# Kernel tuning notes

Hardware: AMD Instinct MI355X
Metric: run time of the kernel (lower is better)

The kernel has to match this reference:

```python
import jax, jax.numpy as jnp
import numpy as np

V = [642, 2562, 10242]
NGT = 8000
NSAMP = 4000
CHAM_W = [3000.0, 3000.0, 3000.0]
LAP_C = [0.2, 1.0, 1.0]
CHAM_OPP = 0.55
W_LAP, W_MOVE, W_EDGE, W_NORM = 1500.0, 50.0, 359.0, 0.5


def _normalize(x, axis=-1):
    n = jnp.linalg.norm(x, axis=axis, keepdims=True)
    return x / jnp.maximum(n, 1e-12)


def _mse(a, b):
    return jnp.mean((a - b) ** 2)


def _sample_points(verts, faces, n, key):
    # uniform face pick + uniform barycentric (sqrt trick), matches sample_point_cloud
    kf, kb = jax.random.split(key)
    fidx = jax.random.randint(kf, (n,), 0, faces.shape[0])
    tri = verts[faces[fidx]]  # [n,3,3]
    uv = jax.random.uniform(kb, (n, 2), dtype=verts.dtype)
    r1 = jnp.sqrt(uv[:, 0]); r2 = uv[:, 1]
    w = jnp.stack([1.0 - r1, r1 * (1.0 - r2), r1 * r2], axis=1)  # [n,3]
    return jnp.einsum('nk,nkd->nd', w, tri)


def _chamfer(gt, pred):
    # squared pairwise distances [B,Ng,Np]
    d = (jnp.sum(gt ** 2, -1)[:, :, None] + jnp.sum(pred ** 2, -1)[:, None, :]
         - 2.0 * jnp.einsum('bnd,bmd->bnm', gt, pred))
    dist1 = jnp.min(d, 2); idx1 = jnp.argmin(d, 2)  # gt -> nearest pred
    dist2 = jnp.min(d, 1); idx2 = jnp.argmin(d, 1)  # pred -> nearest gt
    return dist1, dist2, idx1, idx2


def _laplace_coord(x, lap):
    # x [B,n,3], lap [n,10]: 8 neighbor idx (-1 invalid), self idx, count
    idx = lap[:, :8]
    mask = idx < 0
    safe = jnp.where(mask, 0, idx)
    v = x[:, safe]  # [B,n,8,3]
    v = jnp.where(mask[None, :, :, None], 0.0, v)
    cnt = lap[:, -1].astype(x.dtype)
    return x - v.sum(2) / cnt[None, :, None]


def _block(gt, gtn, pred, pred_bef, lap, edges, faces, key, cham_w, lap_c, block_idx):
    samp = _sample_points(pred[0], faces, NSAMP, key)[None]
    sample_pred = jnp.concatenate([pred, samp], 1)
    d1, d2, _i1, i2 = _chamfer(gt, sample_pred)
    chamfer = cham_w * (jnp.mean(d1) + CHAM_OPP * jnp.mean(d2))
    e = _normalize(pred[:, edges[:, 0]] - pred[:, edges[:, 1]], 2)
    nn = jnp.take_along_axis(gtn, i2[..., None], axis=1)  # nearest gt normal per pred pt
    nrm = _normalize(nn[:, edges[:, 0]], 2)
    normal = jnp.mean(jnp.abs(jnp.sum(e * nrm, 2)))
    edge = _mse(pred[:, edges[:, 0]], pred[:, edges[:, 1]]) * 3.0
    lap_l = lap_c * _mse(_laplace_coord(pred_bef, lap), _laplace_coord(pred, lap)) * 3.0
    move = lap_c * _mse(pred_bef, pred) * 3.0 if block_idx > 0 else 0.0
    return chamfer, normal, edge, lap_l, move


def setup_inputs() -> dict:
    key = jax.random.key(0)
    ks = jax.random.split(key, 8)
    inp = {}
    inp['gt_points'] = jax.random.normal(ks[0], (1, NGT, 3), jnp.float32)
    inp['gt_normals'] = _normalize(jax.random.normal(ks[1], (1, NGT, 3), jnp.float32), 2)
    for i, v in enumerate(V):
        kp, kb, ke, kf, kl = jax.random.split(ks[2 + i], 5)
        pc = jax.random.normal(kp, (1, v, 3), jnp.float32)
        inp[f'pred_coord_{i}'] = pc
        inp[f'pred_before_{i}'] = pc + 0.1 * jax.random.normal(kb, (1, v, 3), jnp.float32)
        inp[f'edges_{i}'] = jax.random.randint(ke, (3 * v, 2), 0, v, dtype=jnp.int32)
        inp[f'faces_{i}'] = jax.random.randint(kf, (2 * v, 3), 0, v, dtype=jnp.int32)
        nbr = jax.random.randint(kl, (v, 8), 0, v, dtype=jnp.int32)
        valid = (nbr % 7) != 0
        valid = valid.at[:, 0].set(True)  # count >= 1
        cnt = valid.sum(1).astype(jnp.int32)
        nbr_m = jnp.where(valid, nbr, -1)
        self_idx = jnp.arange(v, dtype=jnp.int32)[:, None]
        inp[f'lap_idx_{i}'] = jnp.concatenate([nbr_m, self_idx, cnt[:, None]], 1)
    return inp


def reference(gt_points, gt_normals,
              pred_coord_0, pred_before_0, edges_0, faces_0, lap_idx_0,
              pred_coord_1, pred_before_1, edges_1, faces_1, lap_idx_1,
              pred_coord_2, pred_before_2, edges_2, faces_2, lap_idx_2):
    skey = jax.random.key(42)
    preds = [pred_coord_0, pred_coord_1, pred_coord_2]
    befs = [pred_before_0, pred_before_1, pred_before_2]
    edges = [edges_0, edges_1, edges_2]
    faces = [faces_0, faces_1, faces_2]
    laps = [lap_idx_0, lap_idx_1, lap_idx_2]
    ch = nl = el = ll = ml = 0.0
    for i in range(3):
        c, n, e, l, m = _block(gt_points, gt_normals, preds[i], befs[i], laps[i],
                               edges[i], faces[i], jax.random.fold_in(skey, i),
                               CHAM_W[i], LAP_C[i], i)
        ch += c; nl += n; el += e; ll += l; ml += m
    loss = ch + W_LAP * ll + W_MOVE * ml + W_EDGE * el + W_NORM * nl
    return loss
```

## Files before the change

kernel.cpp:

```cpp
#include <hip/hip_runtime.h>
#include <stdint.h>

#define NGT 8000
#define NSAMP 4000
#define QT 8
#define QB 2048
#define CH 128

struct Params {
  const float* gt;
  const float* gtn;
  const float* pred[3];
  const float* bef[3];
  const int*   edges[3];
  const int*   faces[3];
  const int*   lap[3];
  float* S[3];
  unsigned int* mb1[3];
  unsigned long long* mb2a[3];
  unsigned int* mb2b[3];
  float* acc;
  unsigned int* counter;
  unsigned int* init_base;
  int init_words;
  int prep_init_blocks;
  int v[3], M[3], E[3], F[3];
  int cseg[10];
  int cnc[9];
  int fseg[13];
};

__device__ __forceinline__ unsigned int ford(float f){
  unsigned int b = __float_as_uint(f);
  return b ^ ((b >> 31) ? 0xFFFFFFFFu : 0x80000000u);
}
__device__ __forceinline__ float funord(unsigned int u){
  unsigned int b = u ^ ((u >> 31) ? 0x80000000u : 0xFFFFFFFFu);
  return __uint_as_float(b);
}

__device__ __forceinline__ uint32_t rotl32(uint32_t x, int d){ return (x<<d)|(x>>(32-d)); }

__device__ __forceinline__ void tf2x32(uint32_t k0, uint32_t k1, uint32_t c0, uint32_t c1,
                                       uint32_t& o0, uint32_t& o1){
  uint32_t ks2 = k0 ^ k1 ^ 0x1BD11BDAu;
  uint32_t x0 = c0 + k0, x1 = c1 + k1;
  x0+=x1; x1=rotl32(x1,13); x1^=x0;
  x0+=x1; x1=rotl32(x1,15); x1^=x0;
  x0+=x1; x1=rotl32(x1,26); x1^=x0;
  x0+=x1; x1=rotl32(x1, 6); x1^=x0;
  x0+=k1; x1+=ks2+1u;
  x0+=x1; x1=rotl32(x1,17); x1^=x0;
  x0+=x1; x1=rotl32(x1,29); x1^=x0;
  x0+=x1; x1=rotl32(x1,16); x1^=x0;
  x0+=x1; x1=rotl32(x1,24); x1^=x0;
  x0+=ks2; x1+=k0+2u;
  x0+=x1; x1=rotl32(x1,13); x1^=x0;
  x0+=x1; x1=rotl32(x1,15); x1^=x0;
  x0+=x1; x1=rotl32(x1,26); x1^=x0;
  x0+=x1; x1=rotl32(x1, 6); x1^=x0;
  x0+=k0; x1+=k1+3u;
  x0+=x1; x1=rotl32(x1,17); x1^=x0;
  x0+=x1; x1=rotl32(x1,29); x1^=x0;
  x0+=x1; x1=rotl32(x1,16); x1^=x0;
  x0+=x1; x1=rotl32(x1,24); x1^=x0;
  x0+=k1; x1+=ks2+4u;
  x0+=x1; x1=rotl32(x1,13); x1^=x0;
  x0+=x1; x1=rotl32(x1,15); x1^=x0;
  x0+=x1; x1=rotl32(x1,26); x1^=x0;
  x0+=x1; x1=rotl32(x1, 6); x1^=x0;
  x0+=ks2; x1+=k0+5u;
  o0=x0; o1=x1;
}

__device__ __forceinline__ uint32_t rbits(uint32_t k0, uint32_t k1, uint32_t idx, uint32_t total){
  uint32_t half = total>>1, o0, o1;
  if (idx < half){ tf2x32(k0,k1, idx, idx+half, o0, o1); return o0; }
  tf2x32(k0,k1, idx-half, idx, o0, o1); return o1;
}

__global__ __launch_bounds__(256) void prep_kernel(Params p){
  int b = blockIdx.x;
  int t = threadIdx.x;
  if (b < p.prep_init_blocks){
    int wdi = b*256 + t;
    if (wdi < p.init_words)
      p.init_base[wdi] = (wdi < 64) ? 0u : 0xFFFFFFFFu;
    return;
  }
  int rem = b - p.prep_init_blocks;
  int i = rem >> 4;
  int s = ((rem & 15) << 8) + t;
  if (s >= NSAMP) return;
  uint32_t bk0, bk1; tf2x32(0u, 42u, 0u, (uint32_t)i, bk0, bk1);
  uint32_t ka0,kb0,ka1,kb1;
  tf2x32(bk0,bk1, 0u,2u, ka0,kb0);
  tf2x32(bk0,bk1, 1u,3u, ka1,kb1);
  uint32_t fb = rbits(ka0,ka1,(uint32_t)s, NSAMP);
  uint32_t fidx = fb % (uint32_t)p.F[i];
  uint32_t u0b = rbits(kb0,kb1, 2u*(uint32_t)s,    2u*NSAMP);
  uint32_t u1b = rbits(kb0,kb1, 2u*(uint32_t)s+1u, 2u*NSAMP);
  float u0 = __uint_as_float((u0b>>9)|0x3F800000u) - 1.0f;
  float u1 = __uint_as_float((u1b>>9)|0x3F800000u) - 1.0f;
  float r1 = sqrtf(u0);
  float w0 = 1.0f - r1, w1 = r1*(1.0f-u1), w2 = r1*u1;
  const int* f = p.faces[i] + 3*(int)fidx;
  const float* pr = p.pred[i];
  int va=f[0], vb=f[1], vc=f[2];
  float* dst = p.S[i] + 3*s;
  dst[0] = w0*pr[3*va+0] + w1*pr[3*vb+0] + w2*pr[3*vc+0];
  dst[1] = w0*pr[3*va+1] + w1*pr[3*vb+1] + w2*pr[3*vc+1];
  dst[2] = w0*pr[3*va+2] + w1*pr[3*vb+2] + w2*pr[3*vc+2];
}

__device__ __forceinline__ float dist_e(const float4 g, float qx, float qy, float qz){
  return fmaf(g.x,qx, fmaf(g.y,qy, fmaf(g.z,qz, g.w)));
}

__device__ __forceinline__ void scan_min(const float4* __restrict__ tile, int lim,
    const float* qx, const float* qy, const float* qz, float* best)
{
  int k = 0;
  int lim8 = lim & ~7;
  for (; k < lim8; k += 8){
    float4 g0=tile[k+0],g1=tile[k+1],g2=tile[k+2],g3=tile[k+3];
    float4 g4=tile[k+4],g5=tile[k+5],g6=tile[k+6],g7=tile[k+7];
    #pragma unroll
    for (int q=0;q<QT;q++){
      float d0=dist_e(g0,qx[q],qy[q],qz[q]);
      float d1=dist_e(g1,qx[q],qy[q],qz[q]);
      float d2=dist_e(g2,qx[q],qy[q],qz[q]);
      float d3=dist_e(g3,qx[q],qy[q],qz[q]);
      float d4=dist_e(g4,qx[q],qy[q],qz[q]);
      float d5=dist_e(g5,qx[q],qy[q],qz[q]);
      float d6=dist_e(g6,qx[q],qy[q],qz[q]);
      float d7=dist_e(g7,qx[q],qy[q],qz[q]);
      float m = fminf(fminf(best[q], d0), d1);
      m = fminf(fminf(m, d2), d3);
      m = fminf(fminf(m, d4), d5);
      m = fminf(fminf(m, d6), d7);
      best[q] = m;
    }
  }
  for (; k < lim; k++){
    float4 g = tile[k];
    #pragma unroll
    for (int q=0;q<QT;q++)
      best[q] = fminf(best[q], dist_e(g,qx[q],qy[q],qz[q]));
  }
}

__device__ __forceinline__ void scan_argmin(const float4* __restrict__ tile, int lim, int c0,
    const float* qx, const float* qy, const float* qz, float* best, int* bidx)
{
  int k = 0;
  int lim4 = lim & ~3;
  for (; k < lim4; k += 4){
    float4 g0=tile[k+0],g1=tile[k+1],g2=tile[k+2],g3=tile[k+3];
    #pragma unroll
    for (int q=0;q<QT;q++){
      float d0=dist_e(g0,qx[q],qy[q],qz[q]);
      float d1=dist_e(g1,qx[q],qy[q],qz[q]);
      float d2=dist_e(g2,qx[q],qy[q],qz[q]);
      float d3=dist_e(g3,qx[q],qy[q],qz[q]);
      if (d0 < best[q]){ best[q]=d0; bidx[q]=c0+k+0; }
      if (d1 < best[q]){ best[q]=d1; bidx[q]=c0+k+1; }
      if (d2 < best[q]){ best[q]=d2; bidx[q]=c0+k+2; }
      if (d3 < best[q]){ best[q]=d3; bidx[q]=c0+k+3; }
    }
  }
  for (; k < lim; k++){
    float4 g = tile[k];
    #pragma unroll
    for (int q=0;q<QT;q++){
      float d = dist_e(g,qx[q],qy[q],qz[q]);
      if (d < best[q]){ best[q]=d; bidx[q]=c0+k; }
    }
  }
}

__global__ __launch_bounds__(256) void chamfer_kernel(Params p){
  __shared__ float4 tile[CH];
  int b = blockIdx.x;
  int seg = 0;
  #pragma unroll
  for (int s=1;s<9;s++) seg += (b >= p.cseg[s]) ? 1 : 0;
  int rem  = b - p.cseg[seg];
  int nc   = p.cnc[seg];
  int cq   = rem / nc;
  int cc   = rem - cq*nc;
  int role = seg / 3;
  int i    = seg - role*3;
  int t = threadIdx.x;
  int qbase = cq*QB;
  int c0 = cc*CH;
  int v = p.v[i];

  if (role == 0){
    int M = p.M[i];
    int lim = min(M - c0, CH);
    if (t < lim){
      int j = c0 + t;
      const float* src = (j < v) ? (p.pred[i] + 3*j) : (p.S[i] + 3*(j-v));
      float x=src[0], y=src[1], z=src[2];
      tile[t] = make_float4(x,y,z, x*x+y*y+z*z);
    }
    float qx[QT],qy[QT],qz[QT],qs[QT],best[QT];
    #pragma unroll
    for (int k=0;k<QT;k++){
      int q = qbase + t + k*256;
      float x=0.f,y=0.f,z=0.f;
      if (q < NGT){ x=p.gt[3*q]; y=p.gt[3*q+1]; z=p.gt[3*q+2]; }
      qs[k]=x*x+y*y+z*z; qx[k]=-2.f*x; qy[k]=-2.f*y; qz[k]=-2.f*z;
      best[k]=3.4e38f;
    }
    __syncthreads();
    scan_min(tile, lim, qx,qy,qz,best);
    #pragma unroll
    for (int k=0;k<QT;k++){
      int q = qbase + t + k*256;
      if (q < NGT) atomicMin(&p.mb1[i][q], ford(best[k]+qs[k]));
    }
  } else if (role == 1){
    int lim = min(NGT - c0, CH);
    if (t < lim){
      int j = c0 + t;
      float x=p.gt[3*j], y=p.gt[3*j+1], z=p.gt[3*j+2];
      tile[t] = make_float4(x,y,z, x*x+y*y+z*z);
    }
    float qx[QT],qy[QT],qz[QT],qs[QT],best[QT];
    int bidx[QT];
    #pragma unroll
    for (int k=0;k<QT;k++){
      int q = qbase + t + k*256;
      float x=0.f,y=0.f,z=0.f;
      if (q < v){
        const float* src = p.pred[i] + 3*q;
        x=src[0]; y=src[1]; z=src[2];
      }
      qs[k]=x*x+y*y+z*z; qx[k]=-2.f*x; qy[k]=-2.f*y; qz[k]=-2.f*z;
      best[k]=3.4e38f; bidx[k]=0;
    }
    __syncthreads();
    scan_argmin(tile, lim, c0, qx,qy,qz,best,bidx);
    #pragma unroll
    for (int k=0;k<QT;k++){
      int q = qbase + t + k*256;
      if (q < v){
        unsigned long long pk = ((unsigned long long)ford(best[k]+qs[k])<<32) | (unsigned int)bidx[k];
        atomicMin(&p.mb2a[i][q], pk);
      }
    }
  } else {
    int lim = min(NGT - c0, CH);
    if (t < lim){
      int j = c0 + t;
      float x=p.gt[3*j], y=p.gt[3*j+1], z=p.gt[3*j+2];
      tile[t] = make_float4(x,y,z, x*x+y*y+z*z);
    }
    float qx[QT],qy[QT],qz[QT],qs[QT],best[QT];
    #pragma unroll
    for (int k=0;k<QT;k++){
      int q = qbase + t + k*256;
      float x=0.f,y=0.f,z=0.f;
      if (q < NSAMP){
        const float* src = p.S[i] + 3*q;
        x=src[0]; y=src[1]; z=src[2];
      }
      qs[k]=x*x+y*y+z*z; qx[k]=-2.f*x; qy[k]=-2.f*y; qz[k]=-2.f*z;
      best[k]=3.4e38f;
    }
    __syncthreads();
    scan_min(tile, lim, qx,qy,qz,best);
    #pragma unroll
    for (int k=0;k<QT;k++){
      int q = qbase + t + k*256;
      if (q < NSAMP) atomicMin(&p.mb2b[i][q], ford(best[k]+qs[k]));
    }
  }
}

__global__ __launch_bounds__(256) void finish_kernel(Params p, float* out){
  __shared__ float red[256];
  int b = blockIdx.x;
  int seg = 0;
  #pragma unroll
  for (int s=1;s<12;s++) seg += (b >= p.fseg[s]) ? 1 : 0;
  int rem = b - p.fseg[seg];
  int z = seg / 3;
  int i = seg - 3*z;
  int tid = threadIdx.x;
  int gidx = rem*256 + tid;

  if (z == 0){
    int M = p.M[i], v = p.v[i];
    float val = 0.f;
    if (gidx < M){
      if (gidx < v) val = funord((unsigned int)(p.mb2a[i][gidx]>>32));
      else          val = funord(p.mb2b[i][gidx-v]);
    }
    red[tid] = val; __syncthreads();
    for (int s=128;s>0;s>>=1){ if (tid<s) red[tid]+=red[tid+s]; __syncthreads(); }
    if (tid==0 && red[0]!=0.f) atomicAdd(&p.acc[8*i+1], red[0]);
  } else if (z == 1){
    float val = 0.f;
    if (gidx < NGT) val = funord(p.mb1[i][gidx]);
    red[tid] = val; __syncthreads();
    for (int s=128;s>0;s>>=1){ if (tid<s) red[tid]+=red[tid+s]; __syncthreads(); }
    if (tid==0 && red[0]!=0.f) atomicAdd(&p.acc[8*i+0], red[0]);
  } else if (z == 2){
    int E = p.E[i];
    float sq = 0.f, ad = 0.f;
    if (gidx < E){
      int e0 = p.edges[i][2*gidx], e1 = p.edges[i][2*gidx+1];
      const float* pr = p.pred[i];
      float dx = pr[3*e0+0]-pr[3*e1+0];
      float dy = pr[3*e0+1]-pr[3*e1+1];
      float dz = pr[3*e0+2]-pr[3*e1+2];
      sq = dx*dx+dy*dy+dz*dz;
      float inv = 1.0f / fmaxf(sqrtf(sq), 1e-12f);
      int g = (int)(unsigned int)p.mb2a[i][e0];
      float nx = p.gtn[3*g+0], ny = p.gtn[3*g+1], nz = p.gtn[3*g+2];
      float invg = 1.0f / fmaxf(sqrtf(nx*nx+ny*ny+nz*nz), 1e-12f);
      ad = fabsf((dx*nx+dy*ny+dz*nz)*inv*invg);
    }
    red[tid] = ad; __syncthreads();
    for (int s=128;s>0;s>>=1){ if (tid<s) red[tid]+=red[tid+s]; __syncthreads(); }
    if (tid==0 && red[0]!=0.f) atomicAdd(&p.acc[8*i+2], red[0]);
    __syncthreads();
    red[tid] = sq; __syncthreads();
    for (int s=128;s>0;s>>=1){ if (tid<s) red[tid]+=red[tid+s]; __syncthreads(); }
    if (tid==0 && red[0]!=0.f) atomicAdd(&p.acc[8*i+3], red[0]);
  } else {
    int v = p.v[i];
    float lsq = 0.f, msq = 0.f;
    if (gidx < v){
      const int* L = p.lap[i] + 10*gidx;
      const float* B = p.bef[i];
      const float* R = p.pred[i];
      float cnt = (float)L[9];
      float sb0=0,sb1=0,sb2=0, sp0=0,sp1=0,sp2=0;
      #pragma unroll
      for (int k=0;k<8;k++){
        int id = L[k];
        if (id >= 0){
          sb0 += B[3*id+0]; sb1 += B[3*id+1]; sb2 += B[3*id+2];
          sp0 += R[3*id+0]; sp1 += R[3*id+1]; sp2 += R[3*id+2];
        }
      }
      float lb0 = B[3*gidx+0] - sb0/cnt, lb1 = B[3*gidx+1] - sb1/cnt, lb2 = B[3*gidx+2] - sb2/cnt;
      float lp0 = R[3*gidx+0] - sp0/cnt, lp1 = R[3*gidx+1] - sp1/cnt, lp2 = R[3*gidx+2] - sp2/cnt;
      float d0=lb0-lp0, d1=lb1-lp1, d2=lb2-lp2;
      lsq = d0*d0+d1*d1+d2*d2;
      float m0=B[3*gidx+0]-R[3*gidx+0], m1=B[3*gidx+1]-R[3*gidx+1], m2=B[3*gidx+2]-R[3*gidx+2];
      msq = m0*m0+m1*m1+m2*m2;
    }
    red[tid] = lsq; __syncthreads();
    for (int s=128;s>0;s>>=1){ if (tid<s) red[tid]+=red[tid+s]; __syncthreads(); }
    if (tid==0 && red[0]!=0.f) atomicAdd(&p.acc[8*i+4], red[0]);
    __syncthreads();
    red[tid] = msq; __syncthreads();
    for (int s=128;s>0;s>>=1){ if (tid<s) red[tid]+=red[tid+s]; __syncthreads(); }
    if (tid==0 && red[0]!=0.f) atomicAdd(&p.acc[8*i+5], red[0]);
  }

  __syncthreads();
  if (tid == 0){
    __threadfence();
    unsigned int total = gridDim.x;
    unsigned int old = atomicAdd(p.counter, 1u);
    if (old == total-1){
      __threadfence();
      const float CHAMW[3] = {3000.0f, 3000.0f, 3000.0f};
      const float LAPC[3]  = {0.2f, 1.0f, 1.0f};
      float loss = 0.0f;
      for (int m=0;m<3;m++){
        float a0 = __hip_atomic_load(&p.acc[8*m+0], __ATOMIC_RELAXED, __HIP_MEMORY_SCOPE_AGENT);
        float a1 = __hip_atomic_load(&p.acc[8*m+1], __ATOMIC_RELAXED, __HIP_MEMORY_SCOPE_AGENT);
        float a2 = __hip_atomic_load(&p.acc[8*m+2], __ATOMIC_RELAXED, __HIP_MEMORY_SCOPE_AGENT);
        float a3 = __hip_atomic_load(&p.acc[8*m+3], __ATOMIC_RELAXED, __HIP_MEMORY_SCOPE_AGENT);
        float a4 = __hip_atomic_load(&p.acc[8*m+4], __ATOMIC_RELAXED, __HIP_MEMORY_SCOPE_AGENT);
        float a5 = __hip_atomic_load(&p.acc[8*m+5], __ATOMIC_RELAXED, __HIP_MEMORY_SCOPE_AGENT);
        float ch = CHAMW[m]*(a0/(float)NGT + 0.55f*a1/(float)p.M[m]);
        float nl = a2/(float)p.E[m];
        float el = a3/(float)p.E[m];
        float ll = LAPC[m]*a4/(float)p.v[m];
        float ml = (m>0) ? LAPC[m]*a5/(float)p.v[m] : 0.0f;
        loss += ch + 1500.0f*ll + 50.0f*ml + 359.0f*el + 0.5f*nl;
      }
      out[0] = loss;
    }
  }
}

extern "C" void kernel_launch(void* const* d_in, const int* in_sizes, int n_in,
                              void* d_out, int out_size, void* d_ws, size_t ws_size,
                              hipStream_t stream) {
  Params p;
  p.gt  = (const float*)d_in[0];
  p.gtn = (const float*)d_in[1];
  for (int i=0;i<3;i++){
    p.pred[i]  = (const float*)d_in[2+5*i];
    p.bef[i]   = (const float*)d_in[3+5*i];
    p.edges[i] = (const int*)  d_in[4+5*i];
    p.faces[i] = (const int*)  d_in[5+5*i];
    p.lap[i]   = (const int*)  d_in[6+5*i];
    p.v[i] = in_sizes[2+5*i]/3;
    p.E[i] = in_sizes[4+5*i]/2;
    p.F[i] = in_sizes[5+5*i]/3;
    p.M[i] = p.v[i] + NSAMP;
  }
  unsigned int* base = (unsigned int*)d_ws;
  p.acc = (float*)base;
  p.counter = base + 32;
  p.init_base = base;
  unsigned int* w = base + 64;
  for (int i=0;i<3;i++){ p.mb1[i]  = w; w += NGT; }
  for (int i=0;i<3;i++){ p.mb2a[i] = (unsigned long long*)w; w += 2*p.v[i]; }
  for (int i=0;i<3;i++){ p.mb2b[i] = w; w += NSAMP; }
  p.init_words = (int)(w - base);
  for (int i=0;i<3;i++){ p.S[i] = (float*)w; w += NSAMP*3; }

  int cnq[9];
  for (int i=0;i<3;i++){
    cnq[0+i] = (NGT + QB-1)/QB;           p.cnc[0+i] = (p.M[i] + CH-1)/CH;
    cnq[3+i] = (p.v[i] + QB-1)/QB;        p.cnc[3+i] = (NGT + CH-1)/CH;
    cnq[6+i] = (NSAMP + QB-1)/QB;         p.cnc[6+i] = (NGT + CH-1)/CH;
  }
  p.cseg[0] = 0;
  for (int s=0;s<9;s++) p.cseg[s+1] = p.cseg[s] + cnq[s]*p.cnc[s];

  int fn[12];
  for (int i=0;i<3;i++){
    fn[0+i] = (p.M[i] + 255)/256;
    fn[3+i] = (NGT + 255)/256;
    fn[6+i] = (p.E[i] + 255)/256;
    fn[9+i] = (p.v[i] + 255)/256;
  }
  p.fseg[0] = 0;
  for (int s=0;s<12;s++) p.fseg[s+1] = p.fseg[s] + fn[s];

  int initB = (p.init_words + 255)/256;
  p.prep_init_blocks = initB;

  prep_kernel   <<<dim3(initB + 3*16), 256, 0, stream>>>(p);
  chamfer_kernel<<<dim3(p.cseg[9]),    256, 0, stream>>>(p);
  finish_kernel <<<dim3(p.fseg[12]),   256, 0, stream>>>(p, (float*)d_out);
}
```

Baseline: 152.1 us.

## Replace chamfer atomicMin reductions with per-block partial buffers and a reduce kernel

Each chamfer block now writes its partial minima (or packed distance/index) to a dedicated slot in workspace instead of issuing global atomicMin. A new reduce kernel takes the min across chunks per query and folds the sum into the accumulators, which also removes the min-buffer init and two finish-kernel segments. The chunk size rises from 128 to 160, giving fewer partials per query. This trades atomic contention and init work for an extra kernel launch and more global-memory traffic, and it falls back to the old path when the workspace is too small.

```diff
diff --git a/kernel.cpp b/kernel.cpp
--- a/kernel.cpp
+++ b/kernel.cpp
@@ -5,7 +5,7 @@
 #define NSAMP 4000
 #define QT 8
 #define QB 2048
-#define CH 128
+#define CH 160
 
 struct Params {
   const float* gt;
@@ -16,6 +16,9 @@
   const int*   faces[3];
   const int*   lap[3];
   float* S[3];
+  float* pf;
+  unsigned long long* pu;
+  unsigned int* gidx[3];
   unsigned int* mb1[3];
   unsigned long long* mb2a[3];
   unsigned int* mb2b[3];
@@ -24,9 +27,11 @@
   unsigned int* init_base;
   int init_words;
   int prep_init_blocks;
+  int part;
   int v[3], M[3], E[3], F[3];
   int cseg[10];
   int cnc[9];
+  int rseg[10];
   int fseg[13];
 };
 
@@ -179,6 +184,7 @@
   }
 }
 
+template<int PART>
 __global__ __launch_bounds__(256) void chamfer_kernel(Params p){
   __shared__ float4 tile[CH];
   int b = blockIdx.x;
@@ -216,10 +222,19 @@
     }
     __syncthreads();
     scan_min(tile, lim, qx,qy,qz,best);
-    #pragma unroll
-    for (int k=0;k<QT;k++){
-      int q = qbase + t + k*256;
-      if (q < NGT) atomicMin(&p.mb1[i][q], ford(best[k]+qs[k]));
+    if (PART){
+      float* dst = p.pf + (size_t)b*2048;
+      #pragma unroll
+      for (int k=0;k<QT;k++){
+        int q = qbase + t + k*256;
+        if (q < NGT) dst[t + k*256] = best[k]+qs[k];
+      }
+    } else {
+      #pragma unroll
+      for (int k=0;k<QT;k++){
+        int q = qbase + t + k*256;
+        if (q < NGT) atomicMin(&p.mb1[i][q], ford(best[k]+qs[k]));
+      }
     }
   } else if (role == 1){
     int lim = min(NGT - c0, CH);
@@ -243,12 +258,24 @@
     }
     __syncthreads();
     scan_argmin(tile, lim, c0, qx,qy,qz,best,bidx);
-    #pragma unroll
-    for (int k=0;k<QT;k++){
-      int q = qbase + t + k*256;
-      if (q < v){
-        unsigned long long pk = ((unsigned long long)ford(best[k]+qs[k])<<32) | (unsigned int)bidx[k];
-        atomicMin(&p.mb2a[i][q], pk);
+    if (PART){
+      unsigned long long* dst = p.pu + (size_t)(b - p.cseg[3])*2048;
+      #pragma unroll
+      for (int k=0;k<QT;k++){
+        int q = qbase + t + k*256;
+        if (q < v){
+          unsigned long long pk = ((unsigned long long)ford(best[k]+qs[k])<<32) | (unsigned int)bidx[k];
+          dst[t + k*256] = pk;
+        }
+      }
+    } else {
+      #pragma unroll
+      for (int k=0;k<QT;k++){
+        int q = qbase + t + k*256;
+        if (q < v){
+          unsigned long long pk = ((unsigned long long)ford(best[k]+qs[k])<<32) | (unsigned int)bidx[k];
+          atomicMin(&p.mb2a[i][q], pk);
+        }
       }
     }
   } else {
@@ -272,12 +299,69 @@
     }
     __syncthreads();
     scan_min(tile, lim, qx,qy,qz,best);
-    #pragma unroll
-    for (int k=0;k<QT;k++){
-      int q = qbase + t + k*256;
-      if (q < NSAMP) atomicMin(&p.mb2b[i][q], ford(best[k]+qs[k]));
-    }
-  }
+    if (PART){
+      int nu = p.cseg[6] - p.cseg[3];
+      float* dst = p.pf + (size_t)(b - nu)*2048;
+      #pragma unroll
+      for (int k=0;k<QT;k++){
+        int q = qbase + t + k*256;
+        if (q < NSAMP) dst[t + k*256] = best[k]+qs[k];
+      }
+    } else {
+      #pragma unroll
+      for (int k=0;k<QT;k++){
+        int q = qbase + t + k*256;
+        if (q < NSAMP) atomicMin(&p.mb2b[i][q], ford(best[k]+qs[k]));
+      }
+    }
+  }
+}
+
+__global__ __launch_bounds__(256) void reduce_kernel(Params p){
+  __shared__ float red[256];
+  int b = blockIdx.x;
+  int seg = 0;
+  #pragma unroll
+  for (int s=1;s<9;s++) seg += (b >= p.rseg[s]) ? 1 : 0;
+  int rem = b - p.rseg[seg];
+  int role = seg / 3;
+  int i = seg - 3*role;
+  int t = threadIdx.x;
+  int q = rem*256 + t;
+  int cq = q >> 11, slot = q & 2047;
+  float val = 0.f;
+
+  if (role == 0){
+    int nc = p.cnc[i];
+    const float* src = p.pf + (size_t)(p.cseg[i] + cq*nc)*2048 + slot;
+    float m = 3.4e38f;
+    for (int cc=0; cc<nc; cc++) m = fminf(m, src[(size_t)cc*2048]);
+    if (q < NGT) val = m;
+  } else if (role == 1){
+    int nc = p.cnc[3+i];
+    const unsigned long long* src = p.pu + (size_t)(p.cseg[3+i] - p.cseg[3] + cq*nc)*2048 + slot;
+    unsigned long long m = ~0ull;
+    for (int cc=0; cc<nc; cc++){
+      unsigned long long x = src[(size_t)cc*2048];
+      if (x < m) m = x;
+    }
+    if (q < p.v[i]){
+      p.gidx[i][q] = (unsigned int)m;
+      val = funord((unsigned int)(m >> 32));
+    }
+  } else {
+    int nc = p.cnc[6+i];
+    int nu = p.cseg[6] - p.cseg[3];
+    const float* src = p.pf + (size_t)(p.cseg[6+i] + cq*nc - nu)*2048 + slot;
+    float m = 3.4e38f;
+    for (int cc=0; cc<nc; cc++) m = fminf(m, src[(size_t)cc*2048]);
+    if (q < NSAMP) val = m;
+  }
+
+  red[t] = val; __syncthreads();
+  for (int s=128;s>0;s>>=1){ if (t<s) red[t]+=red[t+s]; __syncthreads(); }
+  if (t==0 && red[0]!=0.f)
+    atomicAdd(&p.acc[8*i + ((role==0)?0:1)], red[0]);
 }
 
 __global__ __launch_bounds__(256) void finish_kernel(Params p, float* out){
@@ -319,7 +403,7 @@
       float dz = pr[3*e0+2]-pr[3*e1+2];
       sq = dx*dx+dy*dy+dz*dz;
       float inv = 1.0f / fmaxf(sqrtf(sq), 1e-12f);
-      int g = (int)(unsigned int)p.mb2a[i][e0];
+      int g = p.part ? (int)p.gidx[i][e0] : (int)(unsigned int)p.mb2a[i][e0];
       float nx = p.gtn[3*g+0], ny = p.gtn[3*g+1], nz = p.gtn[3*g+2];
       float invg = 1.0f / fmaxf(sqrtf(nx*nx+ny*ny+nz*nz), 1e-12f);
       ad = fabsf((dx*nx+dy*ny+dz*nz)*inv*invg);
@@ -410,30 +494,63 @@
     p.F[i] = in_sizes[5+5*i]/3;
     p.M[i] = p.v[i] + NSAMP;
   }
+
+  int cnq[9];
+  for (int i=0;i<3;i++){
+    cnq[0+i] = (NGT + QB-1)/QB;           p.cnc[0+i] = (p.M[i] + CH-1)/CH;
+    cnq[3+i] = (p.v[i] + QB-1)/QB;        p.cnc[3+i] = (NGT + CH-1)/CH;
+    cnq[6+i] = (NSAMP + QB-1)/QB;         p.cnc[6+i] = (NGT + CH-1)/CH;
+  }
+  p.cseg[0] = 0;
+  for (int s=0;s<9;s++) p.cseg[s+1] = p.cseg[s] + cnq[s]*p.cnc[s];
+  int nu = p.cseg[6] - p.cseg[3];
+  int nf = p.cseg[3] + (p.cseg[9] - p.cseg[6]);
+
+  size_t part_words = 64
+      + (size_t)(p.v[0]+p.v[1]+p.v[2])
+      + (size_t)3*NSAMP*3
+      + 2
+      + (size_t)nu*2048*2
+      + (size_t)nf*2048;
+  int part = (ws_size >= (part_words + 64)*sizeof(unsigned int)) ? 1 : 0;
+  p.part = part;
+
   unsigned int* base = (unsigned int*)d_ws;
   p.acc = (float*)base;
   p.counter = base + 32;
   p.init_base = base;
   unsigned int* w = base + 64;
-  for (int i=0;i<3;i++){ p.mb1[i]  = w; w += NGT; }
-  for (int i=0;i<3;i++){ p.mb2a[i] = (unsigned long long*)w; w += 2*p.v[i]; }
-  for (int i=0;i<3;i++){ p.mb2b[i] = w; w += NSAMP; }
-  p.init_words = (int)(w - base);
-  for (int i=0;i<3;i++){ p.S[i] = (float*)w; w += NSAMP*3; }
-
-  int cnq[9];
+  p.pf = nullptr; p.pu = nullptr;
+  for (int i=0;i<3;i++){ p.gidx[i]=nullptr; p.mb1[i]=nullptr; p.mb2a[i]=nullptr; p.mb2b[i]=nullptr; }
+
+  if (part){
+    for (int i=0;i<3;i++){ p.gidx[i] = w; w += p.v[i]; }
+    for (int i=0;i<3;i++){ p.S[i] = (float*)w; w += NSAMP*3; }
+    if ((w - base) & 1) w++;
+    p.pu = (unsigned long long*)w; w += (size_t)nu*2048*2;
+    p.pf = (float*)w;              w += (size_t)nf*2048;
+    p.init_words = 64;
+  } else {
+    for (int i=0;i<3;i++){ p.mb1[i]  = w; w += NGT; }
+    for (int i=0;i<3;i++){ p.mb2a[i] = (unsigned long long*)w; w += 2*p.v[i]; }
+    for (int i=0;i<3;i++){ p.mb2b[i] = w; w += NSAMP; }
+    p.init_words = (int)(w - base);
+    for (int i=0;i<3;i++){ p.S[i] = (float*)w; w += NSAMP*3; }
+  }
+
+  int rn[9];
   for (int i=0;i<3;i++){
-    cnq[0+i] = (NGT + QB-1)/QB;           p.cnc[0+i] = (p.M[i] + CH-1)/CH;
-    cnq[3+i] = (p.v[i] + QB-1)/QB;        p.cnc[3+i] = (NGT + CH-1)/CH;
-    cnq[6+i] = (NSAMP + QB-1)/QB;         p.cnc[6+i] = (NGT + CH-1)/CH;
-  }
-  p.cseg[0] = 0;
-  for (int s=0;s<9;s++) p.cseg[s+1] = p.cseg[s] + cnq[s]*p.cnc[s];
+    rn[0+i] = (NGT + 255)/256;
+    rn[3+i] = (p.v[i] + 255)/256;
+    rn[6+i] = (NSAMP + 255)/256;
+  }
+  p.rseg[0] = 0;
+  for (int s=0;s<9;s++) p.rseg[s+1] = p.rseg[s] + rn[s];
 
   int fn[12];
   for (int i=0;i<3;i++){
-    fn[0+i] = (p.M[i] + 255)/256;
-    fn[3+i] = (NGT + 255)/256;
+    fn[0+i] = part ? 0 : (p.M[i] + 255)/256;
+    fn[3+i] = part ? 0 : (NGT + 255)/256;
     fn[6+i] = (p.E[i] + 255)/256;
     fn[9+i] = (p.v[i] + 255)/256;
   }
@@ -443,7 +560,12 @@
   int initB = (p.init_words + 255)/256;
   p.prep_init_blocks = initB;
 
-  prep_kernel   <<<dim3(initB + 3*16), 256, 0, stream>>>(p);
-  chamfer_kernel<<<dim3(p.cseg[9]),    256, 0, stream>>>(p);
-  finish_kernel <<<dim3(p.fseg[12]),   256, 0, stream>>>(p, (float*)d_out);
-}
+  prep_kernel<<<dim3(initB + 3*16), 256, 0, stream>>>(p);
+  if (part){
+    chamfer_kernel<1><<<dim3(p.cseg[9]), 256, 0, stream>>>(p);
+    reduce_kernel  <<<dim3(p.rseg[9]),   256, 0, stream>>>(p);
+  } else {
+    chamfer_kernel<0><<<dim3(p.cseg[9]), 256, 0, stream>>>(p);
+  }
+  finish_kernel<<<dim3(p.fseg[12]), 256, 0, stream>>>(p, (float*)d_out);
+}
```

New measurement: 171.1 us. +12.5%, slower.

## Use packed FP32 FMA and min3 in chamfer scans with SoA tiles

Applied to the files above, without the earlier changes.

Switches the shared-memory candidate tile from an array of float4 to four separate x/y/z/norm arrays, so pairs of candidates can be loaded as float2. Distances are then computed two at a time with v_pk_fma_f32, and min reduction uses v_min3_f32, roughly halving the VALU instruction count in the inner loop. The tile size grows from 128 to 160 and launch bounds now request 4 blocks per CU. The changes add register pressure from the duplicated query vectors, and CH depends on host-side segment counts (cnc/cseg), which must match the new value.

```diff
diff --git a/kernel.cpp b/kernel.cpp
--- a/kernel.cpp
+++ b/kernel.cpp
@@ -5,7 +5,9 @@
 #define NSAMP 4000
 #define QT 8
 #define QB 2048
-#define CH 128
+#define CH 160
+
+typedef float f32x2 __attribute__((ext_vector_type(2)));
 
 struct Params {
   const float* gt;
@@ -37,6 +39,17 @@
 __device__ __forceinline__ float funord(unsigned int u){
   unsigned int b = u ^ ((u >> 31) ? 0x80000000u : 0xFFFFFFFFu);
   return __uint_as_float(b);
+}
+
+__device__ __forceinline__ f32x2 pk_fma(f32x2 a, f32x2 b, f32x2 c){
+  f32x2 d;
+  asm("v_pk_fma_f32 %0, %1, %2, %3" : "=v"(d) : "v"(a), "v"(b), "v"(c));
+  return d;
+}
+__device__ __forceinline__ float min3f(float a, float b, float c){
+  float d;
+  asm("v_min3_f32 %0, %1, %2, %3" : "=v"(d) : "v"(a), "v"(b), "v"(c));
+  return d;
 }
 
 __device__ __forceinline__ uint32_t rotl32(uint32_t x, int d){ return (x<<d)|(x>>(32-d)); }
@@ -113,74 +126,100 @@
   dst[2] = w0*pr[3*va+2] + w1*pr[3*vb+2] + w2*pr[3*vc+2];
 }
 
-__device__ __forceinline__ float dist_e(const float4 g, float qx, float qy, float qz){
-  return fmaf(g.x,qx, fmaf(g.y,qy, fmaf(g.z,qz, g.w)));
-}
-
-__device__ __forceinline__ void scan_min(const float4* __restrict__ tile, int lim,
-    const float* qx, const float* qy, const float* qz, float* best)
+
+__device__ __forceinline__ void scan_min_pk(
+    const float* sx, const float* sy, const float* sz, const float* ss, int lim,
+    const f32x2* qx2, const f32x2* qy2, const f32x2* qz2, float* best)
 {
-  int k = 0;
-  int lim8 = lim & ~7;
-  for (; k < lim8; k += 8){
-    float4 g0=tile[k+0],g1=tile[k+1],g2=tile[k+2],g3=tile[k+3];
-    float4 g4=tile[k+4],g5=tile[k+5],g6=tile[k+6],g7=tile[k+7];
-    #pragma unroll
-    for (int q=0;q<QT;q++){
-      float d0=dist_e(g0,qx[q],qy[q],qz[q]);
-      float d1=dist_e(g1,qx[q],qy[q],qz[q]);
-      float d2=dist_e(g2,qx[q],qy[q],qz[q]);
-      float d3=dist_e(g3,qx[q],qy[q],qz[q]);
-      float d4=dist_e(g4,qx[q],qy[q],qz[q]);
-      float d5=dist_e(g5,qx[q],qy[q],qz[q]);
-      float d6=dist_e(g6,qx[q],qy[q],qz[q]);
-      float d7=dist_e(g7,qx[q],qy[q],qz[q]);
-      float m = fminf(fminf(best[q], d0), d1);
-      m = fminf(fminf(m, d2), d3);
-      m = fminf(fminf(m, d4), d5);
-      m = fminf(fminf(m, d6), d7);
-      best[q] = m;
-    }
-  }
-  for (; k < lim; k++){
-    float4 g = tile[k];
-    #pragma unroll
-    for (int q=0;q<QT;q++)
-      best[q] = fminf(best[q], dist_e(g,qx[q],qy[q],qz[q]));
-  }
-}
-
-__device__ __forceinline__ void scan_argmin(const float4* __restrict__ tile, int lim, int c0,
-    const float* qx, const float* qy, const float* qz, float* best, int* bidx)
+  int np = lim >> 1;
+  int m = 0;
+  int np4 = np & ~3;
+  for (; m < np4; m += 4){
+    f32x2 gx0=*(const f32x2*)(sx+2*m),   gx1=*(const f32x2*)(sx+2*m+2),
+          gx2=*(const f32x2*)(sx+2*m+4), gx3=*(const f32x2*)(sx+2*m+6);
+    f32x2 gy0=*(const f32x2*)(sy+2*m),   gy1=*(const f32x2*)(sy+2*m+2),
+          gy2=*(const f32x2*)(sy+2*m+4), gy3=*(const f32x2*)(sy+2*m+6);
+    f32x2 gz0=*(const f32x2*)(sz+2*m),   gz1=*(const f32x2*)(sz+2*m+2),
+          gz2=*(const f32x2*)(sz+2*m+4), gz3=*(const f32x2*)(sz+2*m+6);
+    f32x2 gs0=*(const f32x2*)(ss+2*m),   gs1=*(const f32x2*)(ss+2*m+2),
+          gs2=*(const f32x2*)(ss+2*m+4), gs3=*(const f32x2*)(ss+2*m+6);
+    #pragma unroll
+    for (int q=0;q<QT;q++){
+      f32x2 a0 = pk_fma(gx0, qx2[q], pk_fma(gy0, qy2[q], pk_fma(gz0, qz2[q], gs0)));
+      f32x2 a1 = pk_fma(gx1, qx2[q], pk_fma(gy1, qy2[q], pk_fma(gz1, qz2[q], gs1)));
+      f32x2 a2 = pk_fma(gx2, qx2[q], pk_fma(gy2, qy2[q], pk_fma(gz2, qz2[q], gs2)));
+      f32x2 a3 = pk_fma(gx3, qx2[q], pk_fma(gy3, qy2[q], pk_fma(gz3, qz2[q], gs3)));
+      float b0 = min3f(best[q], a0.x, a0.y);
+      float b1 = min3f(b0,      a1.x, a1.y);
+      float b2 = min3f(b1,      a2.x, a2.y);
+      best[q]  = min3f(b2,      a3.x, a3.y);
+    }
+  }
+  for (; m < np; m++){
+    f32x2 gx=*(const f32x2*)(sx+2*m), gy=*(const f32x2*)(sy+2*m),
+          gz=*(const f32x2*)(sz+2*m), gs=*(const f32x2*)(ss+2*m);
+    #pragma unroll
+    for (int q=0;q<QT;q++){
+      f32x2 a = pk_fma(gx, qx2[q], pk_fma(gy, qy2[q], pk_fma(gz, qz2[q], gs)));
+      best[q] = min3f(best[q], a.x, a.y);
+    }
+  }
+  if (lim & 1){
+    int j = lim - 1;
+    float gx=sx[j], gy=sy[j], gz=sz[j], gs=ss[j];
+    #pragma unroll
+    for (int q=0;q<QT;q++){
+      float d = fmaf(gx,qx2[q].x, fmaf(gy,qy2[q].x, fmaf(gz,qz2[q].x, gs)));
+      best[q] = fminf(best[q], d);
+    }
+  }
+}
+
+__device__ __forceinline__ void scan_argmin_pk(
+    const float* sx, const float* sy, const float* sz, const float* ss, int lim, int c0,
+    const f32x2* qx2, const f32x2* qy2, const f32x2* qz2, float* best, int* bidx)
 {
-  int k = 0;
-  int lim4 = lim & ~3;
-  for (; k < lim4; k += 4){
-    float4 g0=tile[k+0],g1=tile[k+1],g2=tile[k+2],g3=tile[k+3];
-    #pragma unroll
-    for (int q=0;q<QT;q++){
-      float d0=dist_e(g0,qx[q],qy[q],qz[q]);
-      float d1=dist_e(g1,qx[q],qy[q],qz[q]);
-      float d2=dist_e(g2,qx[q],qy[q],qz[q]);
-      float d3=dist_e(g3,qx[q],qy[q],qz[q]);
-      if (d0 < best[q]){ best[q]=d0; bidx[q]=c0+k+0; }
-      if (d1 < best[q]){ best[q]=d1; bidx[q]=c0+k+1; }
-      if (d2 < best[q]){ best[q]=d2; bidx[q]=c0+k+2; }
-      if (d3 < best[q]){ best[q]=d3; bidx[q]=c0+k+3; }
-    }
-  }
-  for (; k < lim; k++){
-    float4 g = tile[k];
-    #pragma unroll
-    for (int q=0;q<QT;q++){
-      float d = dist_e(g,qx[q],qy[q],qz[q]);
-      if (d < best[q]){ best[q]=d; bidx[q]=c0+k; }
-    }
-  }
-}
-
-__global__ __launch_bounds__(256) void chamfer_kernel(Params p){
-  __shared__ float4 tile[CH];
+  int np = lim >> 1;
+  int m = 0;
+  int np2 = np & ~1;
+  for (; m < np2; m += 2){
+    f32x2 gx0=*(const f32x2*)(sx+2*m), gx1=*(const f32x2*)(sx+2*m+2);
+    f32x2 gy0=*(const f32x2*)(sy+2*m), gy1=*(const f32x2*)(sy+2*m+2);
+    f32x2 gz0=*(const f32x2*)(sz+2*m), gz1=*(const f32x2*)(sz+2*m+2);
+    f32x2 gs0=*(const f32x2*)(ss+2*m), gs1=*(const f32x2*)(ss+2*m+2);
+    #pragma unroll
+    for (int q=0;q<QT;q++){
+      f32x2 a0 = pk_fma(gx0, qx2[q], pk_fma(gy0, qy2[q], pk_fma(gz0, qz2[q], gs0)));
+      f32x2 a1 = pk_fma(gx1, qx2[q], pk_fma(gy1, qy2[q], pk_fma(gz1, qz2[q], gs1)));
+      if (a0.x < best[q]){ best[q]=a0.x; bidx[q]=c0+2*m+0; }
+      if (a0.y < best[q]){ best[q]=a0.y; bidx[q]=c0+2*m+1; }
+      if (a1.x < best[q]){ best[q]=a1.x; bidx[q]=c0+2*m+2; }
+      if (a1.y < best[q]){ best[q]=a1.y; bidx[q]=c0+2*m+3; }
+    }
+  }
+  for (; m < np; m++){
+    f32x2 gx=*(const f32x2*)(sx+2*m), gy=*(const f32x2*)(sy+2*m),
+          gz=*(const f32x2*)(sz+2*m), gs=*(const f32x2*)(ss+2*m);
+    #pragma unroll
+    for (int q=0;q<QT;q++){
+      f32x2 a = pk_fma(gx, qx2[q], pk_fma(gy, qy2[q], pk_fma(gz, qz2[q], gs)));
+      if (a.x < best[q]){ best[q]=a.x; bidx[q]=c0+2*m+0; }
+      if (a.y < best[q]){ best[q]=a.y; bidx[q]=c0+2*m+1; }
+    }
+  }
+  if (lim & 1){
+    int j = lim - 1;
+    float gx=sx[j], gy=sy[j], gz=sz[j], gs=ss[j];
+    #pragma unroll
+    for (int q=0;q<QT;q++){
+      float d = fmaf(gx,qx2[q].x, fmaf(gy,qy2[q].x, fmaf(gz,qz2[q].x, gs)));
+      if (d < best[q]){ best[q]=d; bidx[q]=c0+j; }
+    }
+  }
+}
+
+__global__ __launch_bounds__(256, 4) void chamfer_kernel(Params p){
+  __shared__ __align__(16) float sx[CH], sy[CH], sz[CH], ss[CH];
   int b = blockIdx.x;
   int seg = 0;
   #pragma unroll
@@ -203,19 +242,22 @@
       int j = c0 + t;
       const float* src = (j < v) ? (p.pred[i] + 3*j) : (p.S[i] + 3*(j-v));
       float x=src[0], y=src[1], z=src[2];
-      tile[t] = make_float4(x,y,z, x*x+y*y+z*z);
-    }
-    float qx[QT],qy[QT],qz[QT],qs[QT],best[QT];
+      sx[t]=x; sy[t]=y; sz[t]=z; ss[t]=x*x+y*y+z*z;
+    }
+    f32x2 qx2[QT],qy2[QT],qz2[QT];
+    float qs[QT],best[QT];
     #pragma unroll
     for (int k=0;k<QT;k++){
       int q = qbase + t + k*256;
       float x=0.f,y=0.f,z=0.f;
       if (q < NGT){ x=p.gt[3*q]; y=p.gt[3*q+1]; z=p.gt[3*q+2]; }
-      qs[k]=x*x+y*y+z*z; qx[k]=-2.f*x; qy[k]=-2.f*y; qz[k]=-2.f*z;
+      qs[k]=x*x+y*y+z*z;
+      float ax=-2.f*x, ay=-2.f*y, az=-2.f*z;
+      qx2[k]=f32x2{ax,ax}; qy2[k]=f32x2{ay,ay}; qz2[k]=f32x2{az,az};
       best[k]=3.4e38f;
     }
     __syncthreads();
-    scan_min(tile, lim, qx,qy,qz,best);
+    scan_min_pk(sx,sy,sz,ss, lim, qx2,qy2,qz2, best);
     #pragma unroll
     for (int k=0;k<QT;k++){
       int q = qbase + t + k*256;
@@ -226,9 +268,10 @@
     if (t < lim){
       int j = c0 + t;
       float x=p.gt[3*j], y=p.gt[3*j+1], z=p.gt[3*j+2];
-      tile[t] = make_float4(x,y,z, x*x+y*y+z*z);
-    }
-    float qx[QT],qy[QT],qz[QT],qs[QT],best[QT];
+      sx[t]=x; sy[t]=y; sz[t]=z; ss[t]=x*x+y*y+z*z;
+    }
+    f32x2 qx2[QT],qy2[QT],qz2[QT];
+    float qs[QT],best[QT];
     int bidx[QT];
     #pragma unroll
     for (int k=0;k<QT;k++){
@@ -238,11 +281,13 @@
         const float* src = p.pred[i] + 3*q;
         x=src[0]; y=src[1]; z=src[2];
       }
-      qs[k]=x*x+y*y+z*z; qx[k]=-2.f*x; qy[k]=-2.f*y; qz[k]=-2.f*z;
+      qs[k]=x*x+y*y+z*z;
+      float ax=-2.f*x, ay=-2.f*y, az=-2.f*z;
+      qx2[k]=f32x2{ax,ax}; qy2[k]=f32x2{ay,ay}; qz2[k]=f32x2{az,az};
       best[k]=3.4e38f; bidx[k]=0;
     }
     __syncthreads();
-    scan_argmin(tile, lim, c0, qx,qy,qz,best,bidx);
+    scan_argmin_pk(sx,sy,sz,ss, lim, c0, qx2,qy2,qz2, best, bidx);
     #pragma unroll
     for (int k=0;k<QT;k++){
       int q = qbase + t + k*256;
@@ -256,9 +301,10 @@
     if (t < lim){
       int j = c0 + t;
       float x=p.gt[3*j], y=p.gt[3*j+1], z=p.gt[3*j+2];
-      tile[t] = make_float4(x,y,z, x*x+y*y+z*z);
-    }
-    float qx[QT],qy[QT],qz[QT],qs[QT],best[QT];
+      sx[t]=x; sy[t]=y; sz[t]=z; ss[t]=x*x+y*y+z*z;
+    }
+    f32x2 qx2[QT],qy2[QT],qz2[QT];
+    float qs[QT],best[QT];
     #pragma unroll
     for (int k=0;k<QT;k++){
       int q = qbase + t + k*256;
@@ -267,11 +313,13 @@
         const float* src = p.S[i] + 3*q;
         x=src[0]; y=src[1]; z=src[2];
       }
-      qs[k]=x*x+y*y+z*z; qx[k]=-2.f*x; qy[k]=-2.f*y; qz[k]=-2.f*z;
+      qs[k]=x*x+y*y+z*z;
+      float ax=-2.f*x, ay=-2.f*y, az=-2.f*z;
+      qx2[k]=f32x2{ax,ax}; qy2[k]=f32x2{ay,ay}; qz2[k]=f32x2{az,az};
       best[k]=3.4e38f;
     }
     __syncthreads();
-    scan_min(tile, lim, qx,qy,qz,best);
+    scan_min_pk(sx,sy,sz,ss, lim, qx2,qy2,qz2, best);
     #pragma unroll
     for (int k=0;k<QT;k++){
       int q = qbase + t + k*256;
```

Measured after the change: 160.6 us. 5.6% more time.

## Prepack points as padded float4 with norms and scan from global memory

Applied to the files above, without the earlier changes.

The prep kernel now writes padded float4 arrays (xyz plus squared norm) for ground-truth and predicted-plus-sampled points. Padding entries carry a huge norm so they never win the minimum. The chamfer kernel drops its shared-memory tile and __syncthreads and reads these packed arrays straight from global memory, where every thread loads the same addresses. The chunk size grows from 128 to 192 and the scan loop runs a fixed length with no tail loop. In exchange it adds workspace, extra prep work and more redundant global/L1 loads per thread.

```diff
diff --git a/kernel.cpp b/kernel.cpp
--- a/kernel.cpp
+++ b/kernel.cpp
@@ -2,10 +2,12 @@
 #include <stdint.h>
 
 #define NGT 8000
+#define NGTPAD 8064
+#define NCGT 42
 #define NSAMP 4000
 #define QT 8
 #define QB 2048
-#define CH 128
+#define CH 192
 
 struct Params {
   const float* gt;
@@ -16,6 +18,8 @@
   const int*   faces[3];
   const int*   lap[3];
   float* S[3];
+  float* gtpk;
+  float* Ppk[3];
   unsigned int* mb1[3];
   unsigned long long* mb2a[3];
   unsigned int* mb2b[3];
@@ -25,6 +29,8 @@
   int init_words;
   int prep_init_blocks;
   int v[3], M[3], E[3], F[3];
+  int padM[3];
+  int ppB[3];
   int cseg[10];
   int cnc[9];
   int fseg[13];
@@ -88,9 +94,41 @@
       p.init_base[wdi] = (wdi < 64) ? 0u : 0xFFFFFFFFu;
     return;
   }
-  int rem = b - p.prep_init_blocks;
-  int i = rem >> 4;
-  int s = ((rem & 15) << 8) + t;
+  b -= p.prep_init_blocks;
+  if (b < 32){
+    int idx = b*256 + t;
+    if (idx < NGTPAD){
+      float4 o;
+      if (idx < NGT){
+        float x=p.gt[3*idx], y=p.gt[3*idx+1], z=p.gt[3*idx+2];
+        o = make_float4(x,y,z, x*x+y*y+z*z);
+      } else {
+        o = make_float4(0.f,0.f,0.f,3.4e38f);
+      }
+      ((float4*)p.gtpk)[idx] = o;
+    }
+    return;
+  }
+  b -= 32;
+  #pragma unroll
+  for (int i=0;i<3;i++){
+    if (b < p.ppB[i]){
+      int idx = b*256 + t;
+      if (idx < p.padM[i]){
+        int v = p.v[i];
+        if (idx < v){
+          float x=p.pred[i][3*idx], y=p.pred[i][3*idx+1], z=p.pred[i][3*idx+2];
+          ((float4*)p.Ppk[i])[idx] = make_float4(x,y,z, x*x+y*y+z*z);
+        } else if (idx >= v + NSAMP){
+          ((float4*)p.Ppk[i])[idx] = make_float4(0.f,0.f,0.f,3.4e38f);
+        }
+      }
+      return;
+    }
+    b -= p.ppB[i];
+  }
+  int i = b >> 4;
+  int s = ((b & 15) << 8) + t;
   if (s >= NSAMP) return;
   uint32_t bk0, bk1; tf2x32(0u, 42u, 0u, (uint32_t)i, bk0, bk1);
   uint32_t ka0,kb0,ka1,kb1;
@@ -107,80 +145,16 @@
   const int* f = p.faces[i] + 3*(int)fidx;
   const float* pr = p.pred[i];
   int va=f[0], vb=f[1], vc=f[2];
+  float d0 = w0*pr[3*va+0] + w1*pr[3*vb+0] + w2*pr[3*vc+0];
+  float d1 = w0*pr[3*va+1] + w1*pr[3*vb+1] + w2*pr[3*vc+1];
+  float d2 = w0*pr[3*va+2] + w1*pr[3*vb+2] + w2*pr[3*vc+2];
   float* dst = p.S[i] + 3*s;
-  dst[0] = w0*pr[3*va+0] + w1*pr[3*vb+0] + w2*pr[3*vc+0];
-  dst[1] = w0*pr[3*va+1] + w1*pr[3*vb+1] + w2*pr[3*vc+1];
-  dst[2] = w0*pr[3*va+2] + w1*pr[3*vb+2] + w2*pr[3*vc+2];
-}
-
-__device__ __forceinline__ float dist_e(const float4 g, float qx, float qy, float qz){
-  return fmaf(g.x,qx, fmaf(g.y,qy, fmaf(g.z,qz, g.w)));
-}
-
-__device__ __forceinline__ void scan_min(const float4* __restrict__ tile, int lim,
-    const float* qx, const float* qy, const float* qz, float* best)
-{
-  int k = 0;
-  int lim8 = lim & ~7;
-  for (; k < lim8; k += 8){
-    float4 g0=tile[k+0],g1=tile[k+1],g2=tile[k+2],g3=tile[k+3];
-    float4 g4=tile[k+4],g5=tile[k+5],g6=tile[k+6],g7=tile[k+7];
-    #pragma unroll
-    for (int q=0;q<QT;q++){
-      float d0=dist_e(g0,qx[q],qy[q],qz[q]);
-      float d1=dist_e(g1,qx[q],qy[q],qz[q]);
-      float d2=dist_e(g2,qx[q],qy[q],qz[q]);
-      float d3=dist_e(g3,qx[q],qy[q],qz[q]);
-      float d4=dist_e(g4,qx[q],qy[q],qz[q]);
-      float d5=dist_e(g5,qx[q],qy[q],qz[q]);
-      float d6=dist_e(g6,qx[q],qy[q],qz[q]);
-      float d7=dist_e(g7,qx[q],qy[q],qz[q]);
-      float m = fminf(fminf(best[q], d0), d1);
-      m = fminf(fminf(m, d2), d3);
-      m = fminf(fminf(m, d4), d5);
-      m = fminf(fminf(m, d6), d7);
-      best[q] = m;
-    }
-  }
-  for (; k < lim; k++){
-    float4 g = tile[k];
-    #pragma unroll
-    for (int q=0;q<QT;q++)
-      best[q] = fminf(best[q], dist_e(g,qx[q],qy[q],qz[q]));
-  }
-}
-
-__device__ __forceinline__ void scan_argmin(const float4* __restrict__ tile, int lim, int c0,
-    const float* qx, const float* qy, const float* qz, float* best, int* bidx)
-{
-  int k = 0;
-  int lim4 = lim & ~3;
-  for (; k < lim4; k += 4){
-    float4 g0=tile[k+0],g1=tile[k+1],g2=tile[k+2],g3=tile[k+3];
-    #pragma unroll
-    for (int q=0;q<QT;q++){
-      float d0=dist_e(g0,qx[q],qy[q],qz[q]);
-      float d1=dist_e(g1,qx[q],qy[q],qz[q]);
-      float d2=dist_e(g2,qx[q],qy[q],qz[q]);
-      float d3=dist_e(g3,qx[q],qy[q],qz[q]);
-      if (d0 < best[q]){ best[q]=d0; bidx[q]=c0+k+0; }
-      if (d1 < best[q]){ best[q]=d1; bidx[q]=c0+k+1; }
-      if (d2 < best[q]){ best[q]=d2; bidx[q]=c0+k+2; }
-      if (d3 < best[q]){ best[q]=d3; bidx[q]=c0+k+3; }
-    }
-  }
-  for (; k < lim; k++){
-    float4 g = tile[k];
-    #pragma unroll
-    for (int q=0;q<QT;q++){
-      float d = dist_e(g,qx[q],qy[q],qz[q]);
-      if (d < best[q]){ best[q]=d; bidx[q]=c0+k; }
-    }
-  }
-}
+  dst[0]=d0; dst[1]=d1; dst[2]=d2;
+  ((float4*)p.Ppk[i])[p.v[i]+s] = make_float4(d0,d1,d2, d0*d0+d1*d1+d2*d2);
+}
+
 
 __global__ __launch_bounds__(256) void chamfer_kernel(Params p){
-  __shared__ float4 tile[CH];
   int b = blockIdx.x;
   int seg = 0;
   #pragma unroll
@@ -196,53 +170,47 @@
   int c0 = cc*CH;
   int v = p.v[i];
 
+  const float4* __restrict__ Pt;
+  const float4* __restrict__ Qb;
+  int qn, qoff;
   if (role == 0){
-    int M = p.M[i];
-    int lim = min(M - c0, CH);
-    if (t < lim){
-      int j = c0 + t;
-      const float* src = (j < v) ? (p.pred[i] + 3*j) : (p.S[i] + 3*(j-v));
-      float x=src[0], y=src[1], z=src[2];
-      tile[t] = make_float4(x,y,z, x*x+y*y+z*z);
-    }
-    float qx[QT],qy[QT],qz[QT],qs[QT],best[QT];
-    #pragma unroll
-    for (int k=0;k<QT;k++){
-      int q = qbase + t + k*256;
-      float x=0.f,y=0.f,z=0.f;
-      if (q < NGT){ x=p.gt[3*q]; y=p.gt[3*q+1]; z=p.gt[3*q+2]; }
-      qs[k]=x*x+y*y+z*z; qx[k]=-2.f*x; qy[k]=-2.f*y; qz[k]=-2.f*z;
-      best[k]=3.4e38f;
-    }
-    __syncthreads();
-    scan_min(tile, lim, qx,qy,qz,best);
-    #pragma unroll
-    for (int k=0;k<QT;k++){
-      int q = qbase + t + k*256;
-      if (q < NGT) atomicMin(&p.mb1[i][q], ford(best[k]+qs[k]));
-    }
+    Pt = (const float4*)p.Ppk[i]; Qb = (const float4*)p.gtpk;   qn = NGT;   qoff = 0;
   } else if (role == 1){
-    int lim = min(NGT - c0, CH);
-    if (t < lim){
-      int j = c0 + t;
-      float x=p.gt[3*j], y=p.gt[3*j+1], z=p.gt[3*j+2];
-      tile[t] = make_float4(x,y,z, x*x+y*y+z*z);
-    }
-    float qx[QT],qy[QT],qz[QT],qs[QT],best[QT];
+    Pt = (const float4*)p.gtpk;   Qb = (const float4*)p.Ppk[i]; qn = v;     qoff = 0;
+  } else {
+    Pt = (const float4*)p.gtpk;   Qb = (const float4*)p.Ppk[i]; qn = NSAMP; qoff = v;
+  }
+  Pt += c0;
+
+  float qx[QT],qy[QT],qz[QT],qs[QT],best[QT];
+  #pragma unroll
+  for (int k=0;k<QT;k++){
+    int q = qbase + t + k*256;
+    float x=0.f,y=0.f,z=0.f,sv=0.f;
+    if (q < qn){
+      float4 g = Qb[qoff + q];
+      x=g.x; y=g.y; z=g.z; sv=g.w;
+    }
+    qs[k]=sv; qx[k]=-2.f*x; qy[k]=-2.f*y; qz[k]=-2.f*z;
+    best[k]=3.4e38f;
+  }
+
+  if (role == 1){
     int bidx[QT];
     #pragma unroll
-    for (int k=0;k<QT;k++){
-      int q = qbase + t + k*256;
-      float x=0.f,y=0.f,z=0.f;
-      if (q < v){
-        const float* src = p.pred[i] + 3*q;
-        x=src[0]; y=src[1]; z=src[2];
-      }
-      qs[k]=x*x+y*y+z*z; qx[k]=-2.f*x; qy[k]=-2.f*y; qz[k]=-2.f*z;
-      best[k]=3.4e38f; bidx[k]=0;
-    }
-    __syncthreads();
-    scan_argmin(tile, lim, c0, qx,qy,qz,best,bidx);
+    for (int k=0;k<QT;k++) bidx[k]=0;
+    #pragma unroll 4
+    for (int k=0;k<CH;k+=2){
+      float4 g0 = Pt[k];
+      float4 g1 = Pt[k+1];
+      #pragma unroll
+      for (int q=0;q<QT;q++){
+        float d0 = fmaf(g0.x,qx[q], fmaf(g0.y,qy[q], fmaf(g0.z,qz[q], g0.w)));
+        float d1 = fmaf(g1.x,qx[q], fmaf(g1.y,qy[q], fmaf(g1.z,qz[q], g1.w)));
+        if (d0 < best[q]){ best[q]=d0; bidx[q]=c0+k;   }
+        if (d1 < best[q]){ best[q]=d1; bidx[q]=c0+k+1; }
+      }
+    }
     #pragma unroll
     for (int k=0;k<QT;k++){
       int q = qbase + t + k*256;
@@ -252,30 +220,29 @@
       }
     }
   } else {
-    int lim = min(NGT - c0, CH);
-    if (t < lim){
-      int j = c0 + t;
-      float x=p.gt[3*j], y=p.gt[3*j+1], z=p.gt[3*j+2];
-      tile[t] = make_float4(x,y,z, x*x+y*y+z*z);
-    }
-    float qx[QT],qy[QT],qz[QT],qs[QT],best[QT];
-    #pragma unroll
-    for (int k=0;k<QT;k++){
-      int q = qbase + t + k*256;
-      float x=0.f,y=0.f,z=0.f;
-      if (q < NSAMP){
-        const float* src = p.S[i] + 3*q;
-        x=src[0]; y=src[1]; z=src[2];
-      }
-      qs[k]=x*x+y*y+z*z; qx[k]=-2.f*x; qy[k]=-2.f*y; qz[k]=-2.f*z;
-      best[k]=3.4e38f;
-    }
-    __syncthreads();
-    scan_min(tile, lim, qx,qy,qz,best);
-    #pragma unroll
-    for (int k=0;k<QT;k++){
-      int q = qbase + t + k*256;
-      if (q < NSAMP) atomicMin(&p.mb2b[i][q], ford(best[k]+qs[k]));
+    #pragma unroll 8
+    for (int k=0;k<CH;k+=2){
+      float4 g0 = Pt[k];
+      float4 g1 = Pt[k+1];
+      #pragma unroll
+      for (int q=0;q<QT;q++){
+        float d0 = fmaf(g0.x,qx[q], fmaf(g0.y,qy[q], fmaf(g0.z,qz[q], g0.w)));
+        float d1 = fmaf(g1.x,qx[q], fmaf(g1.y,qy[q], fmaf(g1.z,qz[q], g1.w)));
+        best[q] = fminf(fminf(best[q], d0), d1);
+      }
+    }
+    if (role == 0){
+      #pragma unroll
+      for (int k=0;k<QT;k++){
+        int q = qbase + t + k*256;
+        if (q < NGT) atomicMin(&p.mb1[i][q], ford(best[k]+qs[k]));
+      }
+    } else {
+      #pragma unroll
+      for (int k=0;k<QT;k++){
+        int q = qbase + t + k*256;
+        if (q < NSAMP) atomicMin(&p.mb2b[i][q], ford(best[k]+qs[k]));
+      }
     }
   }
 }
@@ -409,6 +376,8 @@
     p.E[i] = in_sizes[4+5*i]/2;
     p.F[i] = in_sizes[5+5*i]/3;
     p.M[i] = p.v[i] + NSAMP;
+    p.padM[i] = ((p.M[i] + CH-1)/CH)*CH;
+    p.ppB[i] = (p.padM[i] + 255)/256;
   }
   unsigned int* base = (unsigned int*)d_ws;
   p.acc = (float*)base;
@@ -420,12 +389,15 @@
   for (int i=0;i<3;i++){ p.mb2b[i] = w; w += NSAMP; }
   p.init_words = (int)(w - base);
   for (int i=0;i<3;i++){ p.S[i] = (float*)w; w += NSAMP*3; }
+  while ((w - base) & 3) w++;
+  p.gtpk = (float*)w; w += NGTPAD*4;
+  for (int i=0;i<3;i++){ p.Ppk[i] = (float*)w; w += (size_t)p.padM[i]*4; }
 
   int cnq[9];
   for (int i=0;i<3;i++){
-    cnq[0+i] = (NGT + QB-1)/QB;           p.cnc[0+i] = (p.M[i] + CH-1)/CH;
-    cnq[3+i] = (p.v[i] + QB-1)/QB;        p.cnc[3+i] = (NGT + CH-1)/CH;
-    cnq[6+i] = (NSAMP + QB-1)/QB;         p.cnc[6+i] = (NGT + CH-1)/CH;
+    cnq[0+i] = (NGT + QB-1)/QB;           p.cnc[0+i] = p.padM[i]/CH;
+    cnq[3+i] = (p.v[i] + QB-1)/QB;        p.cnc[3+i] = NCGT;
+    cnq[6+i] = (NSAMP + QB-1)/QB;         p.cnc[6+i] = NCGT;
   }
   p.cseg[0] = 0;
   for (int s=0;s<9;s++) p.cseg[s+1] = p.cseg[s] + cnq[s]*p.cnc[s];
@@ -442,8 +414,9 @@
 
   int initB = (p.init_words + 255)/256;
   p.prep_init_blocks = initB;
-
-  prep_kernel   <<<dim3(initB + 3*16), 256, 0, stream>>>(p);
-  chamfer_kernel<<<dim3(p.cseg[9]),    256, 0, stream>>>(p);
-  finish_kernel <<<dim3(p.fseg[12]),   256, 0, stream>>>(p, (float*)d_out);
-}
+  int prepB = initB + 32 + p.ppB[0] + p.ppB[1] + p.ppB[2] + 3*16;
+
+  prep_kernel   <<<dim3(prepB),     256, 0, stream>>>(p);
+  chamfer_kernel<<<dim3(p.cseg[9]), 256, 0, stream>>>(p);
+  finish_kernel <<<dim3(p.fseg[12]),256, 0, stream>>>(p, (float*)d_out);
+}
```

New measurement: 162.1 us. 1.07x slower.
